# Performance work log

Measured on AMD Instinct MI355X. Metric: run time of the kernel, lower is better.

## Reference

```python
import jax, jax.numpy as jnp
import numpy as np

EMBED_DIM = 1024
NUM_HEADS = 16
HEAD_DIM = EMBED_DIM // NUM_HEADS


def setup_inputs() -> dict:
    key = jax.random.key(0)
    k_x, k_wqkv, k_bqkv, k_wo, k_bo = jax.random.split(key, 5)
    B, T, C = 8, 1024, EMBED_DIM
    s = 1.0 / np.sqrt(C)
    return {
        "x": jax.random.normal(k_x, (B, T, C), dtype=jnp.float32),
        "W_qkv": jax.random.uniform(k_wqkv, (C, 3 * C), minval=-s, maxval=s, dtype=jnp.float32),
        "b_qkv": jax.random.uniform(k_bqkv, (3 * C,), minval=-s, maxval=s, dtype=jnp.float32),
        "W_out": jax.random.uniform(k_wo, (C, C), minval=-s, maxval=s, dtype=jnp.float32),
        "b_out": jax.random.uniform(k_bo, (C,), minval=-s, maxval=s, dtype=jnp.float32),
    }


def reference(x, W_qkv, b_qkv, W_out, b_out):
    B, T, C = x.shape
    H, D = NUM_HEADS, HEAD_DIM
    qkv = x @ W_qkv + b_qkv                      # [B,T,3C]
    q, k, v = jnp.split(qkv, 3, axis=-1)
    q = q.reshape(B, T, H, D).transpose(0, 2, 1, 3)  # [B,H,T,D]
    k = k.reshape(B, T, H, D).transpose(0, 2, 1, 3)
    v = v.reshape(B, T, H, D).transpose(0, 2, 1, 3)
    scores = jnp.einsum("bhqd,bhkd->bhqk", q, k) / np.sqrt(D).astype(np.float32)
    causal = jnp.tril(jnp.ones((T, T), dtype=bool))
    scores = jnp.where(causal[None, None], scores, -jnp.inf)
    attn = jax.nn.softmax(scores, axis=-1)       # dropout is identity in eval
    out = jnp.einsum("bhqk,bhkd->bhqd", attn, v)
    out = out.transpose(0, 2, 1, 3).reshape(B, T, C)
    return out @ W_out + b_out
```

## Files before the change

kernel.cpp:

```cpp
#include <hip/hip_runtime.h>
#include <hip/hip_bf16.h>
#include <cstdint>

using bf16 = __hip_bfloat16;
typedef short short8 __attribute__((ext_vector_type(8)));
typedef float floatx4 __attribute__((ext_vector_type(4)));

#define QSCALE 0.1803368801111601f

__device__ __forceinline__ void async_load16(const bf16* g, bf16* l) {
    __builtin_amdgcn_global_load_lds(
        (const __attribute__((address_space(1))) uint32_t*)g,
        (__attribute__((address_space(3))) uint32_t*)l, 16, 0, 0);
}

__device__ __forceinline__ void bar_vm4_lgkm0() {
    asm volatile("s_waitcnt vmcnt(4) lgkmcnt(0)\ns_barrier" ::: "memory");
}
__device__ __forceinline__ void bar_vm0_lgkm0() {
    asm volatile("s_waitcnt vmcnt(0) lgkmcnt(0)\ns_barrier" ::: "memory");
}

__device__ __forceinline__ uint32_t pack2(float a, float b) {
    union { bf16 h[2]; uint32_t u; } p;
    p.h[0] = __float2bfloat16(a);
    p.h[1] = __float2bfloat16(b);
    return p.u;
}

__device__ __forceinline__ float fast_exp2(float x) {
    float r;
    asm("v_exp_f32 %0, %1" : "=v"(r) : "v"(x));
    return r;
}

__global__ __launch_bounds__(256)
void cvt_bf16_kernel(const float* __restrict__ in, bf16* __restrict__ out) {
    const int i = (blockIdx.x * 256 + threadIdx.x) * 4;
    const float4 v = *(const float4*)(in + i);
    bf16 o[4] = {__float2bfloat16(v.x), __float2bfloat16(v.y),
                 __float2bfloat16(v.z), __float2bfloat16(v.w)};
    *(ushort4*)(out + i) = *(ushort4*)o;
}

__global__ __launch_bounds__(256)
void transpose_cvt2_kernel(const float* __restrict__ inA, bf16* __restrict__ outA,
                           const float* __restrict__ inB, bf16* __restrict__ outB) {
    __shared__ float tile[32][33];
    const int tx = threadIdx.x & 31, ty = threadIdx.x >> 5;
    const bool isB = blockIdx.x >= 96;
    const float* __restrict__ in = isB ? inB : inA;
    bf16* __restrict__ out = isB ? outB : outA;
    const int C = isB ? 1024 : 3072;
    const int bx = isB ? blockIdx.x - 96 : blockIdx.x;
    const int c0 = bx * 32, r0 = blockIdx.y * 32;
    const int R = 1024;
    #pragma unroll
    for (int i = 0; i < 32; i += 8)
        tile[ty + i][tx] = in[(size_t)(r0 + ty + i) * C + c0 + tx];
    __syncthreads();
    #pragma unroll
    for (int i = 0; i < 32; i += 8)
        out[(size_t)(c0 + ty + i) * R + r0 + tx] = __float2bfloat16(tile[tx][ty + i]);
}

template <int MODE>
__global__ __launch_bounds__(256, 3)
void gemm_bt_kernel(const bf16* __restrict__ A, const bf16* __restrict__ Bt,
                    const float* __restrict__ bias, int K,
                    bf16* __restrict__ q_ws, bf16* __restrict__ k_ws,
                    bf16* __restrict__ vt_ws, float* __restrict__ out, int N) {
    __shared__ bf16 As[3][128 * 32];
    __shared__ bf16 Bs[3][128 * 32];
    const int tid = threadIdx.x;
    const int wave = tid >> 6, lane = tid & 63;
    const int ln = lane & 15, quad = lane >> 4;
    const int wm = wave & 1, wn = wave >> 1;
    const int m0 = blockIdx.y * 128, n0 = blockIdx.x * 128;

    floatx4 acc[4][4] = {};
    const int nkt = K >> 5;

    #pragma unroll
    for (int t = 0; t < 2; ++t) {
        const int k0 = t << 5;
        #pragma unroll
        for (int c = 0; c < 2; ++c) {
            const int e = (c * 256 + tid) * 8;
            async_load16(A + (size_t)(m0 + (e >> 5)) * K + k0 + (e & 31),
                         &As[t][(c * 256 + wave * 64) * 8]);
        }
        #pragma unroll
        for (int c = 0; c < 2; ++c) {
            const int e = (c * 256 + tid) * 8;
            async_load16(Bt + (size_t)(n0 + (e >> 5)) * K + k0 + (e & 31),
                         &Bs[t][(c * 256 + wave * 64) * 8]);
        }
    }

    for (int kt = 0; kt < nkt; ++kt) {
        const int cur = kt % 3;
        if (kt + 1 < nkt) bar_vm4_lgkm0();
        else              bar_vm0_lgkm0();

        if (kt + 2 < nkt) {
            const int nxt = (kt + 2) % 3;
            const int k0 = (kt + 2) << 5;
            #pragma unroll
            for (int c = 0; c < 2; ++c) {
                const int e = (c * 256 + tid) * 8;
                async_load16(A + (size_t)(m0 + (e >> 5)) * K + k0 + (e & 31),
                             &As[nxt][(c * 256 + wave * 64) * 8]);
            }
            #pragma unroll
            for (int c = 0; c < 2; ++c) {
                const int e = (c * 256 + tid) * 8;
                async_load16(Bt + (size_t)(n0 + (e >> 5)) * K + k0 + (e & 31),
                             &Bs[nxt][(c * 256 + wave * 64) * 8]);
            }
        }

        short8 af[4], bfr[4];
        #pragma unroll
        for (int i = 0; i < 4; ++i) {
            af[i]  = *(const short8*)&As[cur][(wm * 64 + i * 16 + ln) * 32 + quad * 8];
            bfr[i] = *(const short8*)&Bs[cur][(wn * 64 + i * 16 + ln) * 32 + quad * 8];
        }
        #pragma unroll
        for (int mi = 0; mi < 4; ++mi)
            #pragma unroll
            for (int ni = 0; ni < 4; ++ni)
                acc[mi][ni] = __builtin_amdgcn_mfma_f32_16x16x32_bf16(
                    af[mi], bfr[ni], acc[mi][ni], 0, 0, 0);
    }

    #pragma unroll
    for (int ni = 0; ni < 4; ++ni) {
        const int col = n0 + wn * 64 + ni * 16 + ln;
        const float bv = bias[col];
        if (MODE == 0) {
            const int which = col >> 10;
            const int cc = col & 1023;
            const int h = cc >> 6, d = cc & 63;
            #pragma unroll
            for (int mi = 0; mi < 4; ++mi) {
                const int rowb = m0 + wm * 64 + mi * 16 + quad * 4;
                if (which == 2) {
                    const int bb = rowb >> 10, t = rowb & 1023;
                    const int tl = t & 63;
                    const int tt = (t & ~63) + ((((tl >> 3) ^ (d & 7)) << 3) | (tl & 7));
                    uint2 w2 = { pack2(acc[mi][ni][0] + bv, acc[mi][ni][1] + bv),
                                 pack2(acc[mi][ni][2] + bv, acc[mi][ni][3] + bv) };
                    *(uint2*)&vt_ws[((size_t)(bb * 16 + h) * 64 + d) * 1024 + tt] = w2;
                } else {
                    bf16* dst = (which == 0) ? q_ws : k_ws;
                    #pragma unroll
                    for (int r = 0; r < 4; ++r) {
                        const int row = rowb + r;
                        const int bb = row >> 10, t = row & 1023;
                        float v = acc[mi][ni][r] + bv;
                        if (which == 0) v *= QSCALE;
                        const int dd = (((d >> 3) ^ (t & 7)) << 3) | (d & 7);
                        dst[((size_t)(bb * 16 + h) * 1024 + t) * 64 + dd] =
                            __float2bfloat16(v);
                    }
                }
            }
        } else {
            #pragma unroll
            for (int mi = 0; mi < 4; ++mi) {
                const int rowb = m0 + wm * 64 + mi * 16 + quad * 4;
                #pragma unroll
                for (int r = 0; r < 4; ++r)
                    out[(size_t)(rowb + r) * N + col] = acc[mi][ni][r] + bv;
            }
        }
    }
}

__global__ __launch_bounds__(256, 3)
void attn_kernel(const bf16* __restrict__ Q, const bf16* __restrict__ K,
                 const bf16* __restrict__ Vt, bf16* __restrict__ O) {
    constexpr int T = 1024;
    __shared__ bf16 Ps[128 * 64];

    const int lid = blockIdx.x + (blockIdx.y << 3);
    const int bh = ((lid & 7) << 4) | ((lid >> 3) & 15);
    const int jt = 7 - (lid >> 7);
    const int q0 = jt << 7;

    const int tid = threadIdx.x;
    const int wave = tid >> 6, lane = tid & 63;
    const int ln = lane & 15, quad = lane >> 4;
    const int b = bh >> 4, h = bh & 15;

    const bf16* Qg = Q + ((size_t)bh * T + q0) * 64;
    const bf16* Kg = K + (size_t)bh * T * 64;
    const bf16* Vg = Vt + (size_t)bh * 64 * T;

    short8 bq[2][2];
    #pragma unroll
    for (int qs = 0; qs < 2; ++qs)
        #pragma unroll
        for (int ks = 0; ks < 2; ++ks) {
            const int row = wave * 16 + qs * 64 + ln;
            const int ch = (ks * 4 + quad) ^ (ln & 7);
            bq[qs][ks] = *(const short8*)(Qg + (size_t)row * 64 + ch * 8);
        }

    floatx4 oacc[2][4] = {};
    float rl[2] = {0.f, 0.f};
    const int qb0 = q0 + wave * 16;
    const int qb1 = qb0 + 64;
    const int nktw = ((qb1 + 15) >> 6) + 1;

    for (int kt = 0; kt < nktw; ++kt) {
        const int k0 = kt << 6;
        const bool tail = (k0 + 63 > qb0);

        floatx4 sacc[2][4] = {};
        __builtin_amdgcn_s_setprio(1);
        #pragma unroll
        for (int nj = 0; nj < 4; ++nj) {
            short8 ak[2];
            #pragma unroll
            for (int ks = 0; ks < 2; ++ks) {
                const int trow = k0 + nj * 16 + ln;
                const int ch = (ks * 4 + quad) ^ (ln & 7);
                ak[ks] = *(const short8*)(Kg + (size_t)trow * 64 + ch * 8);
            }
            #pragma unroll
            for (int qs = 0; qs < 2; ++qs) {
                const int qb = qs ? qb1 : qb0;
                if (k0 + nj * 16 > qb + 15) continue;
                #pragma unroll
                for (int ks = 0; ks < 2; ++ks)
                    sacc[qs][nj] = __builtin_amdgcn_mfma_f32_16x16x32_bf16(
                        ak[ks], bq[qs][ks], sacc[qs][nj], 0, 0, 0);
            }
        }
        __builtin_amdgcn_s_setprio(0);

        if (tail) {
            #pragma unroll
            for (int qs = 0; qs < 2; ++qs) {
                const int qq = (qs ? qb1 : qb0) + ln;
                #pragma unroll
                for (int nj = 0; nj < 4; ++nj)
                    #pragma unroll
                    for (int r = 0; r < 4; ++r) {
                        const int kk = k0 + nj * 16 + quad * 4 + r;
                        if (kk > qq) sacc[qs][nj][r] = -1e30f;
                    }
            }
        }

        #pragma unroll
        for (int qs = 0; qs < 2; ++qs) {
            float rs = 0.f;
            const int qrow = wave * 16 + qs * 64 + ln;
            #pragma unroll
            for (int nj = 0; nj < 4; ++nj) {
                float p[4];
                #pragma unroll
                for (int r = 0; r < 4; ++r) {
                    p[r] = fast_exp2(sacc[qs][nj][r]);
                    rs += p[r];
                }
                const int kcol = nj * 16 + quad * 4;
                const int ch = (kcol >> 3) ^ (qrow & 7);
                uint2 w2 = { pack2(p[0], p[1]), pack2(p[2], p[3]) };
                *(uint2*)&Ps[qrow * 64 + ch * 8 + (kcol & 7)] = w2;
            }
            rl[qs] += rs;
        }

        __builtin_amdgcn_s_setprio(1);
        #pragma unroll
        for (int ks4 = 0; ks4 < 2; ++ks4) {
            short8 bp[2];
            #pragma unroll
            for (int qs = 0; qs < 2; ++qs) {
                const int qrow = wave * 16 + qs * 64 + ln;
                const int chp = (ks4 * 4 + quad) ^ (ln & 7);
                bp[qs] = *(const short8*)&Ps[qrow * 64 + chp * 8];
            }
            #pragma unroll
            for (int dt = 0; dt < 4; ++dt) {
                const int d = dt * 16 + ln;
                const int ch = (ks4 * 4 + quad) ^ (ln & 7);
                const short8 av = *(const short8*)(Vg + (size_t)d * T + k0 + ch * 8);
                #pragma unroll
                for (int qs = 0; qs < 2; ++qs)
                    oacc[qs][dt] = __builtin_amdgcn_mfma_f32_16x16x32_bf16(
                        av, bp[qs], oacc[qs][dt], 0, 0, 0);
            }
        }
        __builtin_amdgcn_s_setprio(0);
    }

    #pragma unroll
    for (int qs = 0; qs < 2; ++qs) {
        float l = rl[qs];
        l += __shfl_xor(l, 16, 64);
        l += __shfl_xor(l, 32, 64);
        const float inv = 1.0f / l;
        const int t = q0 + qs * 64 + wave * 16 + ln;
        const size_t rowb = ((size_t)b * 1024 + t) * 1024 + h * 64;
        #pragma unroll
        for (int dt = 0; dt < 4; ++dt) {
            uint2 w2 = { pack2(oacc[qs][dt][0] * inv, oacc[qs][dt][1] * inv),
                         pack2(oacc[qs][dt][2] * inv, oacc[qs][dt][3] * inv) };
            *(uint2*)&O[rowb + dt * 16 + quad * 4] = w2;
        }
    }
}

extern "C" void kernel_launch(void* const* d_in, const int* in_sizes, int n_in,
                              void* d_out, int out_size, void* d_ws, size_t ws_size,
                              hipStream_t stream) {
    const float* x     = (const float*)d_in[0];
    const float* W_qkv = (const float*)d_in[1];
    const float* b_qkv = (const float*)d_in[2];
    const float* W_out = (const float*)d_in[3];
    const float* b_out = (const float*)d_in[4];
    float* out = (float*)d_out;

    char* ws = (char*)d_ws;
    const size_t MB = 1u << 20;
    bf16* x_bf   = (bf16*)(ws + 0);
    bf16* wqkv_t = (bf16*)(ws + 16 * MB);
    bf16* wout_t = (bf16*)(ws + 22 * MB);
    bf16* q_ws   = (bf16*)(ws + 24 * MB);
    bf16* k_ws   = (bf16*)(ws + 40 * MB);
    bf16* vt_ws  = (bf16*)(ws + 56 * MB);
    bf16* ao_ws  = (bf16*)(ws + 72 * MB);

    cvt_bf16_kernel<<<8192, 256, 0, stream>>>(x, x_bf);
    transpose_cvt2_kernel<<<dim3(128, 32), 256, 0, stream>>>(W_qkv, wqkv_t, W_out, wout_t);

    gemm_bt_kernel<0><<<dim3(24, 64), 256, 0, stream>>>(
        x_bf, wqkv_t, b_qkv, 1024, q_ws, k_ws, vt_ws, nullptr, 3072);

    attn_kernel<<<dim3(8, 128), 256, 0, stream>>>(q_ws, k_ws, vt_ws, ao_ws);

    gemm_bt_kernel<1><<<dim3(8, 64), 256, 0, stream>>>(
        ao_ws, wout_t, b_out, 1024, nullptr, nullptr, nullptr, out, 1024);
}
```

Baseline: 241.0 us.

## Halve attention query tile, fuse prep kernels, swizzle GEMM workgroup order

The attention kernel now gives each workgroup 64 query rows instead of 128, with one 16-row slice per wave. This doubles the grid and allows four workgroups per CU, and it skips K loads for fully masked sub-tiles. Each K/V tile is now reused by fewer query rows, so more K/V traffic goes through cache. The two input-conversion kernels are merged into one launch. The GEMM remaps workgroup IDs with an XCD-aware swizzle so neighbouring tiles share L2.

After: 245.7 us. No clear change (+2.0%).

```diff
diff --git a/kernel.cpp b/kernel.cpp
--- a/kernel.cpp
+++ b/kernel.cpp
@@ -35,26 +35,30 @@
 }
 
 __global__ __launch_bounds__(256)
-void cvt_bf16_kernel(const float* __restrict__ in, bf16* __restrict__ out) {
-    const int i = (blockIdx.x * 256 + threadIdx.x) * 4;
-    const float4 v = *(const float4*)(in + i);
-    bf16 o[4] = {__float2bfloat16(v.x), __float2bfloat16(v.y),
-                 __float2bfloat16(v.z), __float2bfloat16(v.w)};
-    *(ushort4*)(out + i) = *(ushort4*)o;
-}
-
-__global__ __launch_bounds__(256)
-void transpose_cvt2_kernel(const float* __restrict__ inA, bf16* __restrict__ outA,
-                           const float* __restrict__ inB, bf16* __restrict__ outB) {
+void prep_kernel(const float* __restrict__ x, bf16* __restrict__ x_bf,
+                 const float* __restrict__ Wqkv, bf16* __restrict__ wqkv_t,
+                 const float* __restrict__ Wout, bf16* __restrict__ wout_t) {
     __shared__ float tile[32][33];
+    const int bid = blockIdx.x;
+    if (bid < 8192) {
+        const int i = (bid * 256 + threadIdx.x) * 4;
+        const float4 v = *(const float4*)(x + i);
+        bf16 o[4] = {__float2bfloat16(v.x), __float2bfloat16(v.y),
+                     __float2bfloat16(v.z), __float2bfloat16(v.w)};
+        *(ushort4*)(x_bf + i) = *(ushort4*)o;
+        return;
+    }
+    const int idx = bid - 8192;
+    const bool isB = idx >= 3072;
+    const float* __restrict__ in = isB ? Wout : Wqkv;
+    bf16* __restrict__ out = isB ? wout_t : wqkv_t;
+    const int C = isB ? 1024 : 3072;
+    const int i2 = isB ? idx - 3072 : idx;
+    const int bx = isB ? (i2 & 31) : (i2 % 96);
+    const int by = isB ? (i2 >> 5) : (i2 / 96);
+    const int c0 = bx * 32, r0 = by * 32;
+    const int R = 1024;
     const int tx = threadIdx.x & 31, ty = threadIdx.x >> 5;
-    const bool isB = blockIdx.x >= 96;
-    const float* __restrict__ in = isB ? inB : inA;
-    bf16* __restrict__ out = isB ? outB : outA;
-    const int C = isB ? 1024 : 3072;
-    const int bx = isB ? blockIdx.x - 96 : blockIdx.x;
-    const int c0 = bx * 32, r0 = blockIdx.y * 32;
-    const int R = 1024;
     #pragma unroll
     for (int i = 0; i < 32; i += 8)
         tile[ty + i][tx] = in[(size_t)(r0 + ty + i) * C + c0 + tx];
@@ -76,7 +80,10 @@
     const int wave = tid >> 6, lane = tid & 63;
     const int ln = lane & 15, quad = lane >> 4;
     const int wm = wave & 1, wn = wave >> 1;
-    const int m0 = blockIdx.y * 128, n0 = blockIdx.x * 128;
+    const int nwg = gridDim.x * gridDim.y;
+    const int lid0 = blockIdx.x + blockIdx.y * gridDim.x;
+    const int swz = (lid0 & 7) * (nwg >> 3) + (lid0 >> 3);
+    const int m0 = (swz / gridDim.x) * 128, n0 = (swz % gridDim.x) * 128;
 
     floatx4 acc[4][4] = {};
     const int nkt = K >> 5;
@@ -178,16 +185,16 @@
     }
 }
 
-__global__ __launch_bounds__(256, 3)
+__global__ __launch_bounds__(256, 4)
 void attn_kernel(const bf16* __restrict__ Q, const bf16* __restrict__ K,
                  const bf16* __restrict__ Vt, bf16* __restrict__ O) {
     constexpr int T = 1024;
-    __shared__ bf16 Ps[128 * 64];
-
-    const int lid = blockIdx.x + (blockIdx.y << 3);
+    __shared__ bf16 Ps[64 * 64];
+
+    const int lid = blockIdx.x + (blockIdx.y << 4);
     const int bh = ((lid & 7) << 4) | ((lid >> 3) & 15);
-    const int jt = 7 - (lid >> 7);
-    const int q0 = jt << 7;
+    const int jt = 15 - (lid >> 7);
+    const int q0 = jt << 6;
 
     const int tid = threadIdx.x;
     const int wave = tid >> 6, lane = tid & 63;
@@ -198,73 +205,59 @@
     const bf16* Kg = K + (size_t)bh * T * 64;
     const bf16* Vg = Vt + (size_t)bh * 64 * T;
 
-    short8 bq[2][2];
-    #pragma unroll
-    for (int qs = 0; qs < 2; ++qs)
-        #pragma unroll
-        for (int ks = 0; ks < 2; ++ks) {
-            const int row = wave * 16 + qs * 64 + ln;
-            const int ch = (ks * 4 + quad) ^ (ln & 7);
-            bq[qs][ks] = *(const short8*)(Qg + (size_t)row * 64 + ch * 8);
-        }
-
-    floatx4 oacc[2][4] = {};
-    float rl[2] = {0.f, 0.f};
-    const int qb0 = q0 + wave * 16;
-    const int qb1 = qb0 + 64;
-    const int nktw = ((qb1 + 15) >> 6) + 1;
+    short8 bq[2];
+    #pragma unroll
+    for (int ks = 0; ks < 2; ++ks) {
+        const int row = wave * 16 + ln;
+        const int ch = (ks * 4 + quad) ^ (ln & 7);
+        bq[ks] = *(const short8*)(Qg + (size_t)row * 64 + ch * 8);
+    }
+
+    floatx4 oacc[4] = {};
+    float rl = 0.f;
+    const int qb = q0 + wave * 16;
+    const int nktw = jt + 1;
 
     for (int kt = 0; kt < nktw; ++kt) {
         const int k0 = kt << 6;
-        const bool tail = (k0 + 63 > qb0);
-
-        floatx4 sacc[2][4] = {};
+        const bool tail = (k0 + 63 > qb);
+
+        floatx4 sacc[4] = {};
         __builtin_amdgcn_s_setprio(1);
         #pragma unroll
         for (int nj = 0; nj < 4; ++nj) {
-            short8 ak[2];
+            if (k0 + nj * 16 > qb + 15) continue;
             #pragma unroll
             for (int ks = 0; ks < 2; ++ks) {
                 const int trow = k0 + nj * 16 + ln;
                 const int ch = (ks * 4 + quad) ^ (ln & 7);
-                ak[ks] = *(const short8*)(Kg + (size_t)trow * 64 + ch * 8);
-            }
-            #pragma unroll
-            for (int qs = 0; qs < 2; ++qs) {
-                const int qb = qs ? qb1 : qb0;
-                if (k0 + nj * 16 > qb + 15) continue;
+                const short8 ak = *(const short8*)(Kg + (size_t)trow * 64 + ch * 8);
+                sacc[nj] = __builtin_amdgcn_mfma_f32_16x16x32_bf16(
+                    ak, bq[ks], sacc[nj], 0, 0, 0);
+            }
+        }
+        __builtin_amdgcn_s_setprio(0);
+
+        if (tail) {
+            const int qq = qb + ln;
+            #pragma unroll
+            for (int nj = 0; nj < 4; ++nj)
                 #pragma unroll
-                for (int ks = 0; ks < 2; ++ks)
-                    sacc[qs][nj] = __builtin_amdgcn_mfma_f32_16x16x32_bf16(
-                        ak[ks], bq[qs][ks], sacc[qs][nj], 0, 0, 0);
-            }
-        }
-        __builtin_amdgcn_s_setprio(0);
-
-        if (tail) {
-            #pragma unroll
-            for (int qs = 0; qs < 2; ++qs) {
-                const int qq = (qs ? qb1 : qb0) + ln;
-                #pragma unroll
-                for (int nj = 0; nj < 4; ++nj)
-                    #pragma unroll
-                    for (int r = 0; r < 4; ++r) {
-                        const int kk = k0 + nj * 16 + quad * 4 + r;
-                        if (kk > qq) sacc[qs][nj][r] = -1e30f;
-                    }
-            }
-        }
-
-        #pragma unroll
-        for (int qs = 0; qs < 2; ++qs) {
+                for (int r = 0; r < 4; ++r) {
+                    const int kk = k0 + nj * 16 + quad * 4 + r;
+                    if (kk > qq) sacc[nj][r] = -1e30f;
+                }
+        }
+
+        {
             float rs = 0.f;
-            const int qrow = wave * 16 + qs * 64 + ln;
+            const int qrow = wave * 16 + ln;
             #pragma unroll
             for (int nj = 0; nj < 4; ++nj) {
                 float p[4];
                 #pragma unroll
                 for (int r = 0; r < 4; ++r) {
-                    p[r] = fast_exp2(sacc[qs][nj][r]);
+                    p[r] = fast_exp2(sacc[nj][r]);
                     rs += p[r];
                 }
                 const int kcol = nj * 16 + quad * 4;
@@ -272,45 +265,38 @@
                 uint2 w2 = { pack2(p[0], p[1]), pack2(p[2], p[3]) };
                 *(uint2*)&Ps[qrow * 64 + ch * 8 + (kcol & 7)] = w2;
             }
-            rl[qs] += rs;
+            rl += rs;
         }
 
         __builtin_amdgcn_s_setprio(1);
         #pragma unroll
         for (int ks4 = 0; ks4 < 2; ++ks4) {
-            short8 bp[2];
-            #pragma unroll
-            for (int qs = 0; qs < 2; ++qs) {
-                const int qrow = wave * 16 + qs * 64 + ln;
-                const int chp = (ks4 * 4 + quad) ^ (ln & 7);
-                bp[qs] = *(const short8*)&Ps[qrow * 64 + chp * 8];
-            }
+            const int qrow = wave * 16 + ln;
+            const int chp = (ks4 * 4 + quad) ^ (ln & 7);
+            const short8 bp = *(const short8*)&Ps[qrow * 64 + chp * 8];
             #pragma unroll
             for (int dt = 0; dt < 4; ++dt) {
                 const int d = dt * 16 + ln;
                 const int ch = (ks4 * 4 + quad) ^ (ln & 7);
                 const short8 av = *(const short8*)(Vg + (size_t)d * T + k0 + ch * 8);
-                #pragma unroll
-                for (int qs = 0; qs < 2; ++qs)
-                    oacc[qs][dt] = __builtin_amdgcn_mfma_f32_16x16x32_bf16(
-                        av, bp[qs], oacc[qs][dt], 0, 0, 0);
+                oacc[dt] = __builtin_amdgcn_mfma_f32_16x16x32_bf16(
+                    av, bp, oacc[dt], 0, 0, 0);
             }
         }
         __builtin_amdgcn_s_setprio(0);
     }
 
-    #pragma unroll
-    for (int qs = 0; qs < 2; ++qs) {
-        float l = rl[qs];
+    {
+        float l = rl;
         l += __shfl_xor(l, 16, 64);
         l += __shfl_xor(l, 32, 64);
         const float inv = 1.0f / l;
-        const int t = q0 + qs * 64 + wave * 16 + ln;
+        const int t = q0 + wave * 16 + ln;
         const size_t rowb = ((size_t)b * 1024 + t) * 1024 + h * 64;
         #pragma unroll
         for (int dt = 0; dt < 4; ++dt) {
-            uint2 w2 = { pack2(oacc[qs][dt][0] * inv, oacc[qs][dt][1] * inv),
-                         pack2(oacc[qs][dt][2] * inv, oacc[qs][dt][3] * inv) };
+            uint2 w2 = { pack2(oacc[dt][0] * inv, oacc[dt][1] * inv),
+                         pack2(oacc[dt][2] * inv, oacc[dt][3] * inv) };
             *(uint2*)&O[rowb + dt * 16 + quad * 4] = w2;
         }
     }
@@ -336,13 +322,12 @@
     bf16* vt_ws  = (bf16*)(ws + 56 * MB);
     bf16* ao_ws  = (bf16*)(ws + 72 * MB);
 
-    cvt_bf16_kernel<<<8192, 256, 0, stream>>>(x, x_bf);
-    transpose_cvt2_kernel<<<dim3(128, 32), 256, 0, stream>>>(W_qkv, wqkv_t, W_out, wout_t);
+    prep_kernel<<<12288, 256, 0, stream>>>(x, x_bf, W_qkv, wqkv_t, W_out, wout_t);
 
     gemm_bt_kernel<0><<<dim3(24, 64), 256, 0, stream>>>(
         x_bf, wqkv_t, b_qkv, 1024, q_ws, k_ws, vt_ws, nullptr, 3072);
 
-    attn_kernel<<<dim3(8, 128), 256, 0, stream>>>(q_ws, k_ws, vt_ws, ao_ws);
+    attn_kernel<<<dim3(16, 128), 256, 0, stream>>>(q_ws, k_ws, vt_ws, ao_ws);
 
     gemm_bt_kernel<1><<<dim3(8, 64), 256, 0, stream>>>(
         ao_ws, wout_t, b_out, 1024, nullptr, nullptr, nullptr, out, 1024);
```

## Add 256x256-tile QKV GEMM with 512 threads and merge prep kernels

Applied to the files above, without the earlier changes.

Replaces the 128x128 templated QKV GEMM with a dedicated 256x256-tile kernel using 8 waves, double-buffered LDS staged in K-halves with XOR swizzle, interleaved async loads between MFMA groups, and s_setprio around MFMA bursts. The larger tile is meant to raise arithmetic intensity and cut global/L2 traffic for the biggest GEMM. It also fuses the x conversion and weight transpose kernels into one launch to drop a launch. The bigger tile produces fewer blocks (384) and raises register and LDS pressure, which may hurt occupancy and load balance.

After: 241.8 us. About the same (+0.3%).

```diff
diff --git a/kernel.cpp b/kernel.cpp
--- a/kernel.cpp
+++ b/kernel.cpp
@@ -35,26 +35,30 @@
 }
 
 __global__ __launch_bounds__(256)
-void cvt_bf16_kernel(const float* __restrict__ in, bf16* __restrict__ out) {
-    const int i = (blockIdx.x * 256 + threadIdx.x) * 4;
-    const float4 v = *(const float4*)(in + i);
-    bf16 o[4] = {__float2bfloat16(v.x), __float2bfloat16(v.y),
-                 __float2bfloat16(v.z), __float2bfloat16(v.w)};
-    *(ushort4*)(out + i) = *(ushort4*)o;
-}
-
-__global__ __launch_bounds__(256)
-void transpose_cvt2_kernel(const float* __restrict__ inA, bf16* __restrict__ outA,
-                           const float* __restrict__ inB, bf16* __restrict__ outB) {
+void prep_kernel(const float* __restrict__ x, bf16* __restrict__ x_bf,
+                 const float* __restrict__ Wqkv, bf16* __restrict__ wqkv_t,
+                 const float* __restrict__ Wout, bf16* __restrict__ wout_t) {
     __shared__ float tile[32][33];
+    const int bid = blockIdx.x;
+    if (bid < 8192) {
+        const int i = (bid * 256 + threadIdx.x) * 4;
+        const float4 v = *(const float4*)(x + i);
+        bf16 o[4] = {__float2bfloat16(v.x), __float2bfloat16(v.y),
+                     __float2bfloat16(v.z), __float2bfloat16(v.w)};
+        *(ushort4*)(x_bf + i) = *(ushort4*)o;
+        return;
+    }
+    const int idx = bid - 8192;
+    const bool isB = idx >= 3072;
+    const float* __restrict__ in = isB ? Wout : Wqkv;
+    bf16* __restrict__ out = isB ? wout_t : wqkv_t;
+    const int C = isB ? 1024 : 3072;
+    const int i2 = isB ? idx - 3072 : idx;
+    const int bx = isB ? (i2 & 31) : (i2 % 96);
+    const int by = isB ? (i2 >> 5) : (i2 / 96);
+    const int c0 = bx * 32, r0 = by * 32;
+    const int R = 1024;
     const int tx = threadIdx.x & 31, ty = threadIdx.x >> 5;
-    const bool isB = blockIdx.x >= 96;
-    const float* __restrict__ in = isB ? inB : inA;
-    bf16* __restrict__ out = isB ? outB : outA;
-    const int C = isB ? 1024 : 3072;
-    const int bx = isB ? blockIdx.x - 96 : blockIdx.x;
-    const int c0 = bx * 32, r0 = blockIdx.y * 32;
-    const int R = 1024;
     #pragma unroll
     for (int i = 0; i < 32; i += 8)
         tile[ty + i][tx] = in[(size_t)(r0 + ty + i) * C + c0 + tx];
@@ -64,12 +68,154 @@
         out[(size_t)(c0 + ty + i) * R + r0 + tx] = __float2bfloat16(tile[tx][ty + i]);
 }
 
-template <int MODE>
+__device__ __forceinline__ void stage_half(const bf16* __restrict__ g, int row0,
+                                           int t, int kh, bf16* lds_kh,
+                                           int tid, int wave) {
+    #pragma unroll
+    for (int c = 0; c < 2; ++c) {
+        const int e = c * 512 + tid;
+        const int row = e >> 2, pc = e & 3;
+        async_load16(g + (size_t)(row0 + row) * 1024 + t * 64 + kh * 32 + ((pc ^ row) & 3) * 8,
+                     lds_kh + (size_t)(c * 512 + wave * 64) * 8);
+    }
+}
+
+__global__ __launch_bounds__(512, 2)
+void gemm_qkv256_kernel(const bf16* __restrict__ A, const bf16* __restrict__ Bt,
+                        const float* __restrict__ bias,
+                        bf16* __restrict__ q_ws, bf16* __restrict__ k_ws,
+                        bf16* __restrict__ vt_ws) {
+    constexpr int NKT = 16;
+    __shared__ bf16 As[2][2 * 8192];
+    __shared__ bf16 Bs[2][2 * 8192];
+    const int tid = threadIdx.x;
+    const int wave = tid >> 6, lane = tid & 63;
+    const int ln = lane & 15, quad = lane >> 4;
+    const int wm = wave >> 2, wn = wave & 3;
+    const int n0 = blockIdx.x * 256, m0 = blockIdx.y * 256;
+
+    floatx4 acc[8][4] = {};
+
+    stage_half(A,  m0, 0, 0, As[0], tid, wave);
+    stage_half(Bt, n0, 0, 0, Bs[0], tid, wave);
+    stage_half(A,  m0, 0, 1, As[0] + 8192, tid, wave);
+    stage_half(Bt, n0, 0, 1, Bs[0] + 8192, tid, wave);
+
+    for (int t = 0; t < NKT; ++t) {
+        bf16* Asb = As[t & 1];
+        bf16* Bsb = Bs[t & 1];
+        bf16* Asn = As[(t & 1) ^ 1];
+        bf16* Bsn = Bs[(t & 1) ^ 1];
+        const bool more = (t + 1 < NKT);
+        short8 af[4], bq[4];
+
+        if (more) stage_half(A, m0, t + 1, 0, Asn, tid, wave);
+        if (more) asm volatile("s_waitcnt vmcnt(6) lgkmcnt(0)\ns_barrier" ::: "memory");
+        else      asm volatile("s_waitcnt vmcnt(4) lgkmcnt(0)\ns_barrier" ::: "memory");
+        #pragma unroll
+        for (int i = 0; i < 4; ++i) {
+            const int ra = wm * 128 + i * 16 + ln;
+            af[i] = *(const short8*)&Asb[ra * 32 + ((quad ^ ra) & 3) * 8];
+            const int rb = wn * 64 + i * 16 + ln;
+            bq[i] = *(const short8*)&Bsb[rb * 32 + ((quad ^ rb) & 3) * 8];
+        }
+        __builtin_amdgcn_s_setprio(1);
+        #pragma unroll
+        for (int i = 0; i < 4; ++i)
+            #pragma unroll
+            for (int n = 0; n < 4; ++n)
+                acc[i][n] = __builtin_amdgcn_mfma_f32_16x16x32_bf16(
+                    af[i], bq[n], acc[i][n], 0, 0, 0);
+        __builtin_amdgcn_s_setprio(0);
+
+        if (more) stage_half(Bt, n0, t + 1, 0, Bsn, tid, wave);
+        #pragma unroll
+        for (int i = 0; i < 4; ++i) {
+            const int ra = wm * 128 + 64 + i * 16 + ln;
+            af[i] = *(const short8*)&Asb[ra * 32 + ((quad ^ ra) & 3) * 8];
+        }
+        __builtin_amdgcn_s_setprio(1);
+        #pragma unroll
+        for (int i = 0; i < 4; ++i)
+            #pragma unroll
+            for (int n = 0; n < 4; ++n)
+                acc[4 + i][n] = __builtin_amdgcn_mfma_f32_16x16x32_bf16(
+                    af[i], bq[n], acc[4 + i][n], 0, 0, 0);
+        __builtin_amdgcn_s_setprio(0);
+
+        if (more) stage_half(A, m0, t + 1, 1, Asn + 8192, tid, wave);
+        if (more) asm volatile("s_waitcnt vmcnt(6) lgkmcnt(0)\ns_barrier" ::: "memory");
+        else      asm volatile("s_waitcnt vmcnt(0) lgkmcnt(0)\ns_barrier" ::: "memory");
+        #pragma unroll
+        for (int i = 0; i < 4; ++i) {
+            const int ra = wm * 128 + i * 16 + ln;
+            af[i] = *(const short8*)&Asb[8192 + ra * 32 + ((quad ^ ra) & 3) * 8];
+            const int rb = wn * 64 + i * 16 + ln;
+            bq[i] = *(const short8*)&Bsb[8192 + rb * 32 + ((quad ^ rb) & 3) * 8];
+        }
+        __builtin_amdgcn_s_setprio(1);
+        #pragma unroll
+        for (int i = 0; i < 4; ++i)
+            #pragma unroll
+            for (int n = 0; n < 4; ++n)
+                acc[i][n] = __builtin_amdgcn_mfma_f32_16x16x32_bf16(
+                    af[i], bq[n], acc[i][n], 0, 0, 0);
+        __builtin_amdgcn_s_setprio(0);
+
+        if (more) stage_half(Bt, n0, t + 1, 1, Bsn + 8192, tid, wave);
+        #pragma unroll
+        for (int i = 0; i < 4; ++i) {
+            const int ra = wm * 128 + 64 + i * 16 + ln;
+            af[i] = *(const short8*)&Asb[8192 + ra * 32 + ((quad ^ ra) & 3) * 8];
+        }
+        __builtin_amdgcn_s_setprio(1);
+        #pragma unroll
+        for (int i = 0; i < 4; ++i)
+            #pragma unroll
+            for (int n = 0; n < 4; ++n)
+                acc[4 + i][n] = __builtin_amdgcn_mfma_f32_16x16x32_bf16(
+                    af[i], bq[n], acc[4 + i][n], 0, 0, 0);
+        __builtin_amdgcn_s_setprio(0);
+    }
+
+    #pragma unroll
+    for (int ni = 0; ni < 4; ++ni) {
+        const int col = n0 + wn * 64 + ni * 16 + ln;
+        const float bv = bias[col];
+        const int which = col >> 10;
+        const int cc = col & 1023;
+        const int h = cc >> 6, d = cc & 63;
+        #pragma unroll
+        for (int mi = 0; mi < 8; ++mi) {
+            const int rowb = m0 + wm * 128 + mi * 16 + quad * 4;
+            if (which == 2) {
+                const int bb = rowb >> 10, t = rowb & 1023;
+                const int tl = t & 63;
+                const int tt = (t & ~63) + ((((tl >> 3) ^ (d & 7)) << 3) | (tl & 7));
+                uint2 w2 = { pack2(acc[mi][ni][0] + bv, acc[mi][ni][1] + bv),
+                             pack2(acc[mi][ni][2] + bv, acc[mi][ni][3] + bv) };
+                *(uint2*)&vt_ws[((size_t)(bb * 16 + h) * 64 + d) * 1024 + tt] = w2;
+            } else {
+                bf16* dst = (which == 0) ? q_ws : k_ws;
+                #pragma unroll
+                for (int r = 0; r < 4; ++r) {
+                    const int row = rowb + r;
+                    const int bb = row >> 10, t = row & 1023;
+                    float v = acc[mi][ni][r] + bv;
+                    if (which == 0) v *= QSCALE;
+                    const int dd = (((d >> 3) ^ (t & 7)) << 3) | (d & 7);
+                    dst[((size_t)(bb * 16 + h) * 1024 + t) * 64 + dd] =
+                        __float2bfloat16(v);
+                }
+            }
+        }
+    }
+}
+
 __global__ __launch_bounds__(256, 3)
 void gemm_bt_kernel(const bf16* __restrict__ A, const bf16* __restrict__ Bt,
                     const float* __restrict__ bias, int K,
-                    bf16* __restrict__ q_ws, bf16* __restrict__ k_ws,
-                    bf16* __restrict__ vt_ws, float* __restrict__ out, int N) {
+                    float* __restrict__ out, int N) {
     __shared__ bf16 As[3][128 * 32];
     __shared__ bf16 Bs[3][128 * 32];
     const int tid = threadIdx.x;
@@ -138,42 +284,12 @@
     for (int ni = 0; ni < 4; ++ni) {
         const int col = n0 + wn * 64 + ni * 16 + ln;
         const float bv = bias[col];
-        if (MODE == 0) {
-            const int which = col >> 10;
-            const int cc = col & 1023;
-            const int h = cc >> 6, d = cc & 63;
-            #pragma unroll
-            for (int mi = 0; mi < 4; ++mi) {
-                const int rowb = m0 + wm * 64 + mi * 16 + quad * 4;
-                if (which == 2) {
-                    const int bb = rowb >> 10, t = rowb & 1023;
-                    const int tl = t & 63;
-                    const int tt = (t & ~63) + ((((tl >> 3) ^ (d & 7)) << 3) | (tl & 7));
-                    uint2 w2 = { pack2(acc[mi][ni][0] + bv, acc[mi][ni][1] + bv),
-                                 pack2(acc[mi][ni][2] + bv, acc[mi][ni][3] + bv) };
-                    *(uint2*)&vt_ws[((size_t)(bb * 16 + h) * 64 + d) * 1024 + tt] = w2;
-                } else {
-                    bf16* dst = (which == 0) ? q_ws : k_ws;
-                    #pragma unroll
-                    for (int r = 0; r < 4; ++r) {
-                        const int row = rowb + r;
-                        const int bb = row >> 10, t = row & 1023;
-                        float v = acc[mi][ni][r] + bv;
-                        if (which == 0) v *= QSCALE;
-                        const int dd = (((d >> 3) ^ (t & 7)) << 3) | (d & 7);
-                        dst[((size_t)(bb * 16 + h) * 1024 + t) * 64 + dd] =
-                            __float2bfloat16(v);
-                    }
-                }
-            }
-        } else {
-            #pragma unroll
-            for (int mi = 0; mi < 4; ++mi) {
-                const int rowb = m0 + wm * 64 + mi * 16 + quad * 4;
-                #pragma unroll
-                for (int r = 0; r < 4; ++r)
-                    out[(size_t)(rowb + r) * N + col] = acc[mi][ni][r] + bv;
-            }
+        #pragma unroll
+        for (int mi = 0; mi < 4; ++mi) {
+            const int rowb = m0 + wm * 64 + mi * 16 + quad * 4;
+            #pragma unroll
+            for (int r = 0; r < 4; ++r)
+                out[(size_t)(rowb + r) * N + col] = acc[mi][ni][r] + bv;
         }
     }
 }
@@ -336,14 +452,13 @@
     bf16* vt_ws  = (bf16*)(ws + 56 * MB);
     bf16* ao_ws  = (bf16*)(ws + 72 * MB);
 
-    cvt_bf16_kernel<<<8192, 256, 0, stream>>>(x, x_bf);
-    transpose_cvt2_kernel<<<dim3(128, 32), 256, 0, stream>>>(W_qkv, wqkv_t, W_out, wout_t);
-
-    gemm_bt_kernel<0><<<dim3(24, 64), 256, 0, stream>>>(
-        x_bf, wqkv_t, b_qkv, 1024, q_ws, k_ws, vt_ws, nullptr, 3072);
+    prep_kernel<<<12288, 256, 0, stream>>>(x, x_bf, W_qkv, wqkv_t, W_out, wout_t);
+
+    gemm_qkv256_kernel<<<dim3(12, 32), 512, 0, stream>>>(
+        x_bf, wqkv_t, b_qkv, q_ws, k_ws, vt_ws);
 
     attn_kernel<<<dim3(8, 128), 256, 0, stream>>>(q_ws, k_ws, vt_ws, ao_ws);
 
-    gemm_bt_kernel<1><<<dim3(8, 64), 256, 0, stream>>>(
-        ao_ws, wout_t, b_out, 1024, nullptr, nullptr, nullptr, out, 1024);
-}
+    gemm_bt_kernel<<<dim3(8, 64), 256, 0, stream>>>(
+        ao_ws, wout_t, b_out, 1024, out, 1024);
+}
```
